# Optimization experiments

Hardware: AMD Instinct MI355X
Metric: run time of the kernel (lower is better)

Reference implementation:

```python
import jax, jax.numpy as jnp
import numpy as np


def _conv1x1(x, w, b=None):
    # x: [B,C,H,W], w: [O,C]
    y = jnp.einsum('bchw,oc->bohw', x, w)
    if b is not None:
        y = y + b[None, :, None, None]
    return y


def _conv3x3_dilated(x, w, b, dil):
    p = dil  # padding == dilation keeps spatial size for 3x3 kernels
    y = jax.lax.conv_general_dilated(
        x, w, window_strides=(1, 1), padding=((p, p), (p, p)),
        rhs_dilation=(dil, dil), dimension_numbers=('NCHW', 'OIHW', 'NCHW'))
    return y + b[None, :, None, None]


def _upsample2x_align_corners(x):
    # bilinear, align_corners=True, scale factor 2
    B, C, H, W = x.shape
    oh, ow = 2 * H, 2 * W
    ys = jnp.linspace(0.0, H - 1.0, oh)
    xs = jnp.linspace(0.0, W - 1.0, ow)
    y0 = jnp.floor(ys).astype(jnp.int32)
    x0 = jnp.floor(xs).astype(jnp.int32)
    y1 = jnp.minimum(y0 + 1, H - 1)
    x1 = jnp.minimum(x0 + 1, W - 1)
    wy = (ys - y0)[None, None, :, None]
    wx = (xs - x0)[None, None, None, :]
    gt = x[:, :, y0, :]
    gb = x[:, :, y1, :]
    top = gt[:, :, :, x0] * (1 - wx) + gt[:, :, :, x1] * wx
    bot = gb[:, :, :, x0] * (1 - wx) + gb[:, :, :, x1] * wx
    return top * (1 - wy) + bot * wy


def _gr(ftr, ck_w, ck_b, avg_w, max_w, gcn_w):
    # GR module: attention-diagonal graph conv with degree normalization
    B, C, H, W = ftr.shape
    HW = H * W
    # ChannelAttention_diag -> diagonal entries cw: [B, M]
    avg = ftr.mean(axis=(2, 3))
    mx = ftr.max(axis=(2, 3))
    cw = jax.nn.sigmoid(jax.nn.relu(avg @ avg_w.T) + jax.nn.relu(mx @ max_w.T))  # [B,M]
    k = jax.nn.relu(_conv1x1(ftr, ck_w, ck_b)).reshape(B, -1, HW)  # [B,M,HW]
    q = jnp.swapaxes(k, 1, 2)  # [B,HW,M]
    # A = sigmoid(q @ diag(cw) @ k); degree d = rowsum(A)^(-1/2)
    A = jax.nn.sigmoid(jnp.einsum('bim,bm,bmj->bij', q, cw, k))  # [B,HW,HW]
    d = A.sum(axis=2) ** -0.5  # [B,HW]
    P = d[:, :, None] * q  # D^{-1/2} @ q, [B,HW,M]
    X = jnp.swapaxes(ftr.reshape(B, C, HW), 1, 2)  # [B,HW,C]
    PtX = jnp.einsum('bjm,bjc->bmc', P, X)  # [B,M,C]
    LX = X - jnp.einsum('bim,bmc->bic', P, cw[:, :, None] * PtX)
    Y = X + LX @ gcn_w  # GCN (no bias)
    return jnp.swapaxes(Y, 1, 2).reshape(B, C, H, W)


def setup_inputs() -> dict:
    key = jax.random.key(0)
    ks = jax.random.split(key, 20)
    B, C = 64, 1024
    Cq = C // 4  # 256
    Mi = Cq // 2  # 128, ChannelAttention inter channels
    s = 0.02
    inp = {
        'x_cur': jax.random.normal(ks[0], (B, C, 16, 16), jnp.float32),
        'x_lat': jax.random.normal(ks[1], (B, C, 8, 8), jnp.float32),
        'conv_w': jax.random.normal(ks[2], (Cq, C), jnp.float32) * s,
        'conv_b': jax.random.normal(ks[3], (Cq,), jnp.float32) * s,
        'conv1_w': jax.random.normal(ks[4], (C, Cq), jnp.float32) * s,
        'conv1_b': jax.random.normal(ks[5], (C,), jnp.float32) * s,
        'conv3_w': jax.random.normal(ks[6], (C, 3 * Cq), jnp.float32) * s,
        'conv3_b': jax.random.normal(ks[7], (C,), jnp.float32) * s,
        'rate0_w': jax.random.normal(ks[8], (Cq, C, 3, 3), jnp.float32) * s,
        'rate0_b': jax.random.normal(ks[9], (Cq,), jnp.float32) * s,
        'rate1_w': jax.random.normal(ks[10], (Cq, C, 3, 3), jnp.float32) * s,
        'rate1_b': jax.random.normal(ks[11], (Cq,), jnp.float32) * s,
        'rate2_w': jax.random.normal(ks[12], (Cq, C, 3, 3), jnp.float32) * s,
        'rate2_b': jax.random.normal(ks[13], (Cq,), jnp.float32) * s,
        'gr_ck_w': jax.random.normal(ks[14], (Mi, Cq), jnp.float32) * s,
        'gr_ck_b': jax.random.normal(ks[15], (Mi,), jnp.float32) * s,
        'gr_avg_w': jax.random.normal(ks[16], (Mi, Cq), jnp.float32) * s,
        'gr_max_w': jax.random.normal(ks[17], (Mi, Cq), jnp.float32) * s,
        'gr_gcn_w': jax.random.normal(ks[18], (Cq, Cq), jnp.float32) * s,
        'pre': 1,
    }
    return inp


def reference(x_cur, x_lat, conv_w, conv_b, conv1_w, conv1_b, conv3_w, conv3_b,
              rate0_w, rate0_b, rate1_w, rate1_b, rate2_w, rate2_b,
              gr_ck_w, gr_ck_b, gr_avg_w, gr_max_w, gr_gcn_w, pre):
    # pre == 1 path of Graph_aspp.forward
    gr_args = (gr_ck_w, gr_ck_b, gr_avg_w, gr_max_w, gr_gcn_w)
    x_sum = x_cur * _upsample2x_align_corners(x_lat) + x_cur
    f1 = _conv3x3_dilated(x_sum, rate0_w, rate0_b, 1) + _conv1x1(x_sum, conv_w, conv_b)
    x1 = _gr(f1, *gr_args)
    feature = _conv1x1(f1, conv1_w, conv1_b) + x_sum
    f2 = _conv3x3_dilated(feature, rate1_w, rate1_b, 2) + _conv1x1(feature, conv_w, conv_b)
    x2 = _gr(f2, *gr_args)
    feature = _conv1x1(f2, conv1_w, conv1_b) + x_sum
    f3 = _conv3x3_dilated(feature, rate2_w, rate2_b, 4) + _conv1x1(feature, conv_w, conv_b)
    x3 = _gr(f3, *gr_args)
    cat = jnp.concatenate((x1, x2, x3), axis=1)
    return _conv1x1(cat, conv3_w, conv3_b)
```

## Files before the change

### kernel.cpp

```cpp
#include <hip/hip_runtime.h>

typedef unsigned short ushort_t;
typedef unsigned int uint32;
typedef __attribute__((ext_vector_type(8))) unsigned short ushort8;
typedef __attribute__((ext_vector_type(8))) __bf16 bf16x8;
typedef __attribute__((ext_vector_type(4))) float f32x4;

__device__ __forceinline__ ushort_t f2b(float f) {
    union { float f; uint32 u; } v; v.f = f;
    uint32 r = v.u + 0x7fffu + ((v.u >> 16) & 1u);
    return (ushort_t)(r >> 16);
}
__device__ __forceinline__ float b2f(ushort_t b) {
    union { uint32 u; float f; } v; v.u = ((uint32)b) << 16;
    return v.f;
}
__device__ __forceinline__ float sigm(float x) { return 1.f / (1.f + __expf(-x)); }

__device__ __forceinline__ void gload_lds16(const void* g, void* l) {
    __builtin_amdgcn_global_load_lds(
        (__attribute__((address_space(1))) void*)g,
        (__attribute__((address_space(3))) void*)l, 16, 0, 0);
}

constexpr int EPI_RELU  = 1;
constexpr int EPI_FEAT  = 2;
constexpr int EPI_SIG   = 3;
constexpr int EPI_XG    = 4;
constexpr int EPI_NEGCW = 5;
constexpr int EPI_Y     = 6;
constexpr int EPI_OUTT  = 7;

struct GemmP {
    const ushort_t* A; const ushort_t* B;
    const ushort_t* A2; const ushort_t* B2;
    long long aBatch, bBatch, a2Batch, b2Batch;
    int lda, ldb, lda2, ldb2;
    int Ksub, kSplit, dil;
    const float* bias;
    const ushort_t* res; long long resBatch; int ldres;
    ushort_t* obf; long long oBatch; int ldo;
    float* of32;
    const float* cw;
    float* dsum;
    const ushort_t* zpage;
};

__global__ __launch_bounds__(256) void gemm_big(GemmP p) {
    __shared__ __align__(16) ushort_t aT[128 * 64];
    __shared__ __align__(16) ushort_t bT[128 * 64];
    const int tid = threadIdx.x;
    const int z = blockIdx.z;
    const int m0 = blockIdx.x * 128, n0 = blockIdx.y * 128;
    const int lane = tid & 63, wid = tid >> 6;
    const int l15 = lane & 15, l16 = lane >> 4;
    const int wr = wid >> 1, wc = wid & 1;
    const int lrow = lane >> 3;
    const int sgran = (lane & 7) ^ lrow;

    int ayy[4], axx[4];
    const ushort_t* aBase[4];
    const ushort_t* bBase[4];
#pragma unroll
    for (int i = 0; i < 4; ++i) {
        int row = wid * 32 + i * 8 + lrow;
        int m = m0 + row;
        int bb = m >> 8;
        ayy[i] = (m >> 4) & 15; axx[i] = m & 15;
        aBase[i] = p.A + (long long)bb * 262144 + sgran * 8;
        bBase[i] = p.B + (long long)(n0 + row) * p.ldb + sgran * 8;
    }

    f32x4 acc[4][4];
#pragma unroll
    for (int i = 0; i < 4; ++i)
#pragma unroll
        for (int j = 0; j < 4; ++j) acc[i][j] = (f32x4){0.f, 0.f, 0.f, 0.f};

    const int gk0 = z * p.kSplit;
    const int iters = p.Ksub >> 6;
    for (int it = 0; it < iters; ++it) {
        const int gk = gk0 + it * 64;
        const int tap = gk >> 10, kin = gk & 1023;
        int dy = 0, dx = 0;
        if (tap < 9) { int ky = tap / 3; dy = (ky - 1) * p.dil; dx = (tap - ky * 3 - 1) * p.dil; }
#pragma unroll
        for (int i = 0; i < 4; ++i) {
            int iy = ayy[i] + dy, ix = axx[i] + dx;
            bool ok = ((unsigned)iy < 16u) && ((unsigned)ix < 16u);
            const ushort_t* ga = ok ? (aBase[i] + (((iy << 4) + ix) << 10) + kin) : p.zpage;
            gload_lds16(ga, &aT[(wid * 32 + i * 8) * 64]);
        }
#pragma unroll
        for (int i = 0; i < 4; ++i)
            gload_lds16(bBase[i] + gk, &bT[(wid * 32 + i * 8) * 64]);
        asm volatile("s_waitcnt vmcnt(0)" ::: "memory");
        __syncthreads();
#pragma unroll
        for (int ks = 0; ks < 2; ++ks) {
            bf16x8 af[4], bfr[4];
#pragma unroll
            for (int mi = 0; mi < 4; ++mi) {
                int rr = wr * 64 + mi * 16 + l15;
                int cc = (ks * 32 + l16 * 8) ^ ((rr & 7) << 3);
                af[mi] = __builtin_bit_cast(bf16x8, *(const ushort8*)&aT[rr * 64 + cc]);
            }
#pragma unroll
            for (int ni = 0; ni < 4; ++ni) {
                int rr = wc * 64 + ni * 16 + l15;
                int cc = (ks * 32 + l16 * 8) ^ ((rr & 7) << 3);
                bfr[ni] = __builtin_bit_cast(bf16x8, *(const ushort8*)&bT[rr * 64 + cc]);
            }
#pragma unroll
            for (int mi = 0; mi < 4; ++mi)
#pragma unroll
                for (int ni = 0; ni < 4; ++ni)
                    acc[mi][ni] = __builtin_amdgcn_mfma_f32_16x16x32_bf16(af[mi], bfr[ni], acc[mi][ni], 0, 0, 0);
        }
        __syncthreads();
    }
#pragma unroll
    for (int mi = 0; mi < 4; ++mi)
#pragma unroll
        for (int ni = 0; ni < 4; ++ni) {
            int gcol = n0 + wc * 64 + ni * 16 + l15;
            int growb = m0 + wr * 64 + mi * 16 + l16 * 4;
#pragma unroll
            for (int r = 0; r < 4; ++r)
                p.obf[(long long)z * p.oBatch + (long long)(growb + r) * 256 + gcol] =
                    f2b(acc[mi][ni][r]);
        }
}

template<int BM, int BN, int AMODE, int EPI>
__global__ __launch_bounds__(256) void gemm_k(GemmP p) {
    __shared__ __align__(16) ushort_t aT[BM * 64];
    __shared__ __align__(16) ushort_t bT[BN * 64];
    constexpr int APASS = BM / 32, BPASS = BN / 32;
    constexpr int MFRAG = BM / 32, NFRAG = BN / 32;
    const int tid = threadIdx.x;
    const int z = blockIdx.z;
    const int m0 = blockIdx.x * BM, n0 = blockIdx.y * BN;
    const int lane = tid & 63, wid = tid >> 6;
    const int l15 = lane & 15, l16 = lane >> 4;
    const int wr = wid >> 1, wc = wid & 1;
    const int srow = tid >> 3, scol = (tid & 7) * 8;
    const int swcol = scol ^ ((srow & 7) << 3);

    const ushort_t* aptr[APASS];
    const ushort_t* bptr[BPASS];
    const ushort_t* aptr2[APASS];
    const ushort_t* bptr2[BPASS];
#pragma unroll
    for (int pi = 0; pi < APASS; ++pi)
        aptr[pi] = p.A + (long long)z * p.aBatch +
                   (long long)(m0 + pi * 32 + srow) * p.lda + scol;
#pragma unroll
    for (int pi = 0; pi < BPASS; ++pi)
        bptr[pi] = p.B + (long long)z * p.bBatch +
                   (long long)(n0 + pi * 32 + srow) * p.ldb + scol;
    if constexpr (AMODE == 2) {
#pragma unroll
        for (int pi = 0; pi < APASS; ++pi)
            aptr2[pi] = p.A2 + (long long)z * p.a2Batch +
                        (long long)(m0 + pi * 32 + srow) * p.lda2 + scol;
#pragma unroll
        for (int pi = 0; pi < BPASS; ++pi)
            bptr2[pi] = p.B2 + (long long)z * p.b2Batch +
                        (long long)(n0 + pi * 32 + srow) * p.ldb2 + scol;
    }

    f32x4 acc[MFRAG][NFRAG];
#pragma unroll
    for (int i = 0; i < MFRAG; ++i)
#pragma unroll
        for (int j = 0; j < NFRAG; ++j) acc[i][j] = (f32x4){0.f, 0.f, 0.f, 0.f};

    ushort8 ar[APASS], br[BPASS];
    auto ldg = [&](int gk) {
        if (AMODE == 2 && gk >= 256) {
            int g2 = gk - 256;
#pragma unroll
            for (int pi = 0; pi < APASS; ++pi) ar[pi] = *(const ushort8*)(aptr2[pi] + g2);
#pragma unroll
            for (int pi = 0; pi < BPASS; ++pi) br[pi] = *(const ushort8*)(bptr2[pi] + g2);
        } else if constexpr (AMODE == 3) {
#pragma unroll
            for (int pi = 0; pi < APASS; ++pi) {
                ushort8 t8 = *(const ushort8*)(aptr[pi] + gk);
#pragma unroll
                for (int k = 0; k < 8; ++k)
                    t8[k] = f2b(b2f(t8[k]) * p.cw[(z << 7) + gk + scol + k]);
                ar[pi] = t8;
            }
#pragma unroll
            for (int pi = 0; pi < BPASS; ++pi) br[pi] = *(const ushort8*)(bptr[pi] + gk);
        } else {
#pragma unroll
            for (int pi = 0; pi < APASS; ++pi) ar[pi] = *(const ushort8*)(aptr[pi] + gk);
#pragma unroll
            for (int pi = 0; pi < BPASS; ++pi) br[pi] = *(const ushort8*)(bptr[pi] + gk);
        }
    };

    const int gk0 = z * p.kSplit;
    ldg(gk0);
    const int iters = p.Ksub >> 6;
    for (int it = 0; it < iters; ++it) {
#pragma unroll
        for (int pi = 0; pi < APASS; ++pi)
            *(ushort8*)&aT[(pi * 32 + srow) * 64 + swcol] = ar[pi];
#pragma unroll
        for (int pi = 0; pi < BPASS; ++pi)
            *(ushort8*)&bT[(pi * 32 + srow) * 64 + swcol] = br[pi];
        __syncthreads();
        if (it + 1 < iters) ldg(gk0 + (it + 1) * 64);
#pragma unroll
        for (int ks = 0; ks < 2; ++ks) {
            bf16x8 af[MFRAG], bfr[NFRAG];
#pragma unroll
            for (int mi = 0; mi < MFRAG; ++mi) {
                int rr = wr * (BM / 2) + mi * 16 + l15;
                int cc = (ks * 32 + l16 * 8) ^ ((rr & 7) << 3);
                af[mi] = __builtin_bit_cast(bf16x8, *(const ushort8*)&aT[rr * 64 + cc]);
            }
#pragma unroll
            for (int ni = 0; ni < NFRAG; ++ni) {
                int rr = wc * (BN / 2) + ni * 16 + l15;
                int cc = (ks * 32 + l16 * 8) ^ ((rr & 7) << 3);
                bfr[ni] = __builtin_bit_cast(bf16x8, *(const ushort8*)&bT[rr * 64 + cc]);
            }
#pragma unroll
            for (int mi = 0; mi < MFRAG; ++mi)
#pragma unroll
                for (int ni = 0; ni < NFRAG; ++ni)
                    acc[mi][ni] = __builtin_amdgcn_mfma_f32_16x16x32_bf16(af[mi], bfr[ni], acc[mi][ni], 0, 0, 0);
        }
        __syncthreads();
    }

#pragma unroll
    for (int mi = 0; mi < MFRAG; ++mi) {
        if constexpr (EPI == EPI_SIG) {
#pragma unroll
            for (int r = 0; r < 4; ++r) {
                float sv = 0.f;
#pragma unroll
                for (int ni = 0; ni < NFRAG; ++ni) sv += sigm(acc[mi][ni][r]);
                sv += __shfl_xor(sv, 1); sv += __shfl_xor(sv, 2);
                sv += __shfl_xor(sv, 4); sv += __shfl_xor(sv, 8);
                if (l15 == 0) {
                    int grow = m0 + wr * (BM / 2) + mi * 16 + l16 * 4 + r;
                    int q8 = blockIdx.y * 2 + wc;
                    p.dsum[q8 * 16384 + z * 256 + grow] = sv;
                }
            }
        } else {
#pragma unroll
            for (int ni = 0; ni < NFRAG; ++ni) {
                int gcol = n0 + wc * (BN / 2) + ni * 16 + l15;
                int growb = m0 + wr * (BM / 2) + mi * 16 + l16 * 4;
#pragma unroll
                for (int r = 0; r < 4; ++r) {
                    int grow = growb + r;
                    float v = acc[mi][ni][r];
                    if constexpr (EPI == EPI_RELU) {
                        v += p.bias[gcol]; v = fmaxf(v, 0.f);
                        p.obf[(long long)grow * p.ldo + gcol] = f2b(v);
                    } else if constexpr (EPI == EPI_FEAT) {
                        v += p.bias[gcol] + b2f(p.res[(long long)grow * p.ldres + gcol]);
                        p.obf[(long long)grow * p.ldo + gcol] = f2b(v);
                    } else if constexpr (EPI == EPI_XG) {
                        p.obf[(long long)z * p.oBatch + (long long)grow * p.ldo + gcol] = f2b(v);
                    } else if constexpr (EPI == EPI_NEGCW) {
                        v *= -p.cw[z * 128 + gcol];
                        p.obf[(long long)z * p.oBatch + (long long)grow * p.ldo + gcol] = f2b(v);
                    } else if constexpr (EPI == EPI_Y) {
                        v = b2f(p.res[(long long)z * p.resBatch + (long long)grow * p.ldres + gcol]) + v;
                        p.obf[(long long)z * p.oBatch + (long long)grow * p.ldo + gcol] = f2b(v);
                    } else if constexpr (EPI == EPI_OUTT) {
                        v += p.bias[grow];
                        int bb = gcol >> 8, px = gcol & 255;
                        p.of32[((long long)bb * 1024 + grow) * 256 + px] = v;
                    }
                }
            }
        }
    }
}


__global__ void k_combine(const ushort_t* __restrict__ t, const float* __restrict__ fbias_s,
                          ushort_t* __restrict__ f) {
    int idx = blockIdx.x * 256 + threadIdx.x;
    const long long N = 16384ll * 256;
    ushort8 a0 = *(const ushort8*)(t + (long long)idx * 8);
    ushort8 a1 = *(const ushort8*)(t + N + (long long)idx * 8);
    ushort8 a2 = *(const ushort8*)(t + 2 * N + (long long)idx * 8);
    ushort8 a3 = *(const ushort8*)(t + 3 * N + (long long)idx * 8);
    ushort8 a4 = *(const ushort8*)(t + 4 * N + (long long)idx * 8);
    int cb = (idx * 8) & 255;
    ushort8 o;
#pragma unroll
    for (int k = 0; k < 8; ++k)
        o[k] = f2b(b2f(a0[k]) + b2f(a1[k]) + b2f(a2[k]) + b2f(a3[k]) + b2f(a4[k]) + fbias_s[cb + k]);
    *(ushort8*)&f[(long long)idx * 8] = o;
}

__global__ void k_upsum(const float* __restrict__ xc, const float* __restrict__ xl,
                        ushort_t* __restrict__ xs) {
    __shared__ float lat[64 * 64];
    __shared__ ushort_t tile[64 * 258];
    int b = blockIdx.x, c0 = blockIdx.y * 64;
    int t = threadIdx.x;
    for (int i = t; i < 4096; i += 256)
        lat[i] = xl[((long long)(b * 1024 + c0 + (i >> 6))) * 64 + (i & 63)];
    __syncthreads();
    int y = t >> 4, x = t & 15;
    float fy = y * (7.f / 15.f); int y0 = (int)fy; float wy = fy - y0; int y1 = y0 + 1 > 7 ? 7 : y0 + 1;
    float fx = x * (7.f / 15.f); int x0 = (int)fx; float wx = fx - x0; int x1 = x0 + 1 > 7 ? 7 : x0 + 1;
    for (int cc = 0; cc < 64; ++cc) {
        float cur = xc[((long long)(b * 1024 + c0 + cc)) * 256 + t];
        const float* L = &lat[cc * 64];
        float tv = L[y0 * 8 + x0] * (1.f - wx) + L[y0 * 8 + x1] * wx;
        float bv = L[y1 * 8 + x0] * (1.f - wx) + L[y1 * 8 + x1] * wx;
        float up = tv + (bv - tv) * wy;
        tile[cc * 258 + t] = f2b(cur * (1.f + up));
    }
    __syncthreads();
    for (int i = t; i < 16384; i += 256) {
        int px = i >> 6, cc = i & 63;
        xs[((long long)(b * 256 + px)) * 1024 + c0 + cc] = tile[cc * 258 + px];
    }
}

__global__ void k_poolcw(const ushort_t* __restrict__ f,
                         const float* __restrict__ aw, const float* __restrict__ mw,
                         float* __restrict__ cw) {
    __shared__ float sa[256], sm[256];
    int b = blockIdx.x, t = threadIdx.x;
    float s = 0.f, m = -3.4e38f;
    const ushort_t* base = f + (long long)b * 65536 + t;
    for (int px = 0; px < 256; ++px) { float v = b2f(base[px * 256]); s += v; m = fmaxf(m, v); }
    sa[t] = s * (1.f / 256.f);
    sm[t] = m;
    __syncthreads();
    if (t < 128) {
        float s1 = 0.f, s2 = 0.f;
        const float* a = aw + t * 256; const float* w = mw + t * 256;
        for (int c = 0; c < 256; ++c) { s1 += sa[c] * a[c]; s2 += sm[c] * w[c]; }
        s1 = fmaxf(s1, 0.f); s2 = fmaxf(s2, 0.f);
        cw[b * 128 + t] = sigm(s1 + s2);
    }
}

__global__ void k_pscale(const ushort_t* __restrict__ q, const float* __restrict__ dsum8,
                         ushort_t* __restrict__ P, ushort_t* __restrict__ Pt) {
    __shared__ ushort_t t[128][130];
    __shared__ float dd[128];
    int jh = blockIdx.x, b = blockIdx.y;
    int j0 = jh * 128;
    int tid = threadIdx.x;
    if (tid < 128) {
        int pix = b * 256 + j0 + tid;
        float s = 0.f;
#pragma unroll
        for (int qs = 0; qs < 8; ++qs) s += dsum8[qs * 16384 + pix];
        dd[tid] = rsqrtf(s);
    }
    __syncthreads();
    int jr = tid >> 7, m = tid & 127;
    for (int i = 0; i < 64; ++i) {
        int j = i * 2 + jr;
        long long qi = ((long long)(b * 256 + j0 + j)) * 128 + m;
        ushort_t v = f2b(dd[j] * b2f(q[qi]));
        P[qi] = v;
        t[j][m] = v;
    }
    __syncthreads();
    for (int i = 0; i < 64; ++i) {
        int mm = i * 2 + jr;
        Pt[((long long)b << 15) + (mm << 8) + j0 + m] = t[m][mm];
    }
}

__global__ void k_packall(const float* r0, const float* r1, const float* r2,
                          const float* convw, const float* c1w, const float* c3w,
                          const float* ckw, const float* gcnw,
                          const float* rb0, const float* rb1, const float* rb2,
                          const float* cb,
                          ushort_t* wbig3, ushort_t* w1b, ushort_t* w3b,
                          ushort_t* ckb, ushort_t* gcnT, float* fbias,
                          ushort_t* zpage) {
    int blk = blockIdx.x, tid = threadIdx.x;
    if (blk < 768) {
        __shared__ float lw[10240];
        int s = blk >> 8, o = blk & 255;
        const float* rate = s == 0 ? r0 : (s == 1 ? r1 : r2);
        for (int i = tid; i < 9216; i += 256) lw[i] = rate[(long long)o * 9216 + i];
        for (int i = tid; i < 1024; i += 256) lw[9216 + i] = convw[(long long)o * 1024 + i];
        __syncthreads();
        ushort_t* dst = wbig3 + (long long)blk * 10240;
        for (int i = tid; i < 10240; i += 256) {
            int tap = i >> 10, ci = i & 1023;
            float v = (tap < 9) ? lw[ci * 9 + tap] : lw[9216 + ci];
            dst[i] = f2b(v);
        }
        return;
    }
    const int R1 = 262144, R2 = R1 + 786432, R3 = R2 + 32768, R4 = R3 + 65536;
    const int R5 = R4 + 768, R6 = R5 + 128;
    int base = (blk - 768) * 2048 + tid * 8;
#pragma unroll
    for (int k = 0; k < 8; ++k) {
        int i = base + k;
        if (i >= R6) return;
        if (i < R1) w1b[i] = f2b(c1w[i]);
        else if (i < R2) w3b[i - R1] = f2b(c3w[i - R1]);
        else if (i < R3) ckb[i - R2] = f2b(ckw[i - R2]);
        else if (i < R4) {
            int ii = i - R3; int c2 = ii >> 8, c1 = ii & 255;
            gcnT[ii] = f2b(gcnw[c1 * 256 + c2]);
        } else if (i < R5) {
            int ii = i - R4; int s = ii >> 8, t = ii & 255;
            const float* rb = s == 0 ? rb0 : (s == 1 ? rb1 : rb2);
            fbias[ii] = rb[t] + cb[t];
        } else {
            zpage[i - R5] = 0;
        }
    }
}

__global__ void k_sentinel(float* o, int n, float v) {
    int i = blockIdx.x * 256 + threadIdx.x; if (i < n) o[i] = v;
}

extern "C" void kernel_launch(void* const* d_in, const int* in_sizes, int n_in,
                              void* d_out, int out_size, void* d_ws, size_t ws_size,
                              hipStream_t stream) {
    const float* x_cur  = (const float*)d_in[0];
    const float* x_lat  = (const float*)d_in[1];
    const float* conv_w = (const float*)d_in[2];
    const float* conv_b = (const float*)d_in[3];
    const float* conv1_w = (const float*)d_in[4];
    const float* conv1_b = (const float*)d_in[5];
    const float* conv3_w = (const float*)d_in[6];
    const float* conv3_b = (const float*)d_in[7];
    const float* rate_w[3] = {(const float*)d_in[8], (const float*)d_in[10], (const float*)d_in[12]};
    const float* rate_b[3] = {(const float*)d_in[9], (const float*)d_in[11], (const float*)d_in[13]};
    const float* ck_w  = (const float*)d_in[14];
    const float* ck_b  = (const float*)d_in[15];
    const float* avg_w = (const float*)d_in[16];
    const float* max_w = (const float*)d_in[17];
    const float* gcn_w = (const float*)d_in[18];
    float* out = (float*)d_out;

    char* w = (char*)d_ws;
    auto take = [&](size_t bytes) { void* p = (void*)w; w += (bytes + 255) & ~(size_t)255; return p; };
    ushort_t* xsum  = (ushort_t*)take(16384ll * 1024 * 2);
    ushort_t* feat  = (ushort_t*)take(16384ll * 1024 * 2);
    ushort_t* fbuf  = (ushort_t*)take(16384ll * 256 * 2);
    ushort_t* xgt   = (ushort_t*)take(64ll * 256 * 256 * 2);
    ushort_t* qbuf  = (ushort_t*)take(16384ll * 128 * 2);
    ushort_t* Pt    = (ushort_t*)take(64ll * 128 * 256 * 2);
    ushort_t* Pb    = (ushort_t*)take(16384ll * 128 * 2);
    ushort_t* Htn   = (ushort_t*)take(64ll * 256 * 128 * 2);
    ushort_t* wbig3 = (ushort_t*)take(3ll * 256 * 10240 * 2);
    ushort_t* w1b   = (ushort_t*)take(1024ll * 256 * 2);
    ushort_t* w3b   = (ushort_t*)take(1024ll * 768 * 2);
    ushort_t* ckb   = (ushort_t*)take(128ll * 256 * 2);
    ushort_t* gcnT  = (ushort_t*)take(256ll * 256 * 2);
    ushort_t* zpage = (ushort_t*)take(256);
    float*    fbias = (float*)take(3 * 256 * 4);
    float*    cwb   = (float*)take(64 * 128 * 4);
    float*    dsum8 = (float*)take(8ll * 64 * 256 * 4);
    ushort_t* catb  = (ushort_t*)take(16384ll * 768 * 2);
    ushort_t* ftmp  = (ushort_t*)take(5ll * 16384 * 256 * 2);
    size_t need = (size_t)(w - (char*)d_ws);

    if (need > ws_size) {
        float v = 1.0e6f + (float)(ws_size >> 20);
        k_sentinel<<<(out_size + 255) / 256, 256, 0, stream>>>(out, out_size, v);
        return;
    }

    k_packall<<<768 + 561, 256, 0, stream>>>(
        rate_w[0], rate_w[1], rate_w[2], conv_w, conv1_w, conv3_w, ck_w, gcn_w,
        rate_b[0], rate_b[1], rate_b[2], conv_b,
        wbig3, w1b, w3b, ckb, gcnT, fbias, zpage);
    k_upsum<<<dim3(64, 16), 256, 0, stream>>>(x_cur, x_lat, xsum);

    for (int s = 0; s < 3; ++s) {
        {
            GemmP p{};
            p.A = (s == 0) ? xsum : feat;
            p.B = wbig3 + (long long)s * 256 * 10240; p.ldb = 10240;
            p.Ksub = 2048; p.kSplit = 2048; p.dil = 1 << s;
            p.obf = ftmp; p.oBatch = 16384ll * 256;
            p.zpage = zpage;
            gemm_big<<<dim3(128, 2, 5), 256, 0, stream>>>(p);
        }
        k_combine<<<2048, 256, 0, stream>>>(ftmp, fbias + s * 256, fbuf);
        k_poolcw<<<64, 256, 0, stream>>>(fbuf, avg_w, max_w, cwb);
        {
            GemmP p{};
            p.A = fbuf; p.lda = 256; p.B = ckb; p.ldb = 256;
            p.Ksub = 256;
            p.bias = ck_b; p.obf = qbuf; p.ldo = 128;
            gemm_k<64, 64, 0, EPI_RELU><<<dim3(256, 2, 1), 256, 0, stream>>>(p);
        }
        {
            GemmP p{};
            p.A = qbuf; p.aBatch = 32768; p.lda = 128;
            p.B = qbuf; p.bBatch = 32768; p.ldb = 128;
            p.Ksub = 128; p.dsum = dsum8; p.cw = cwb;
            gemm_k<64, 64, 3, EPI_SIG><<<dim3(4, 4, 64), 256, 0, stream>>>(p);
        }
        k_pscale<<<dim3(2, 64), 256, 0, stream>>>(qbuf, dsum8, Pb, Pt);
        {
            GemmP p{};
            p.A = gcnT; p.aBatch = 0;     p.lda = 256;
            p.B = fbuf; p.bBatch = 65536; p.ldb = 256;
            p.Ksub = 256;
            p.obf = xgt; p.oBatch = 65536; p.ldo = 256;
            gemm_k<64, 64, 0, EPI_XG><<<dim3(4, 4, 64), 256, 0, stream>>>(p);
        }
        {
            GemmP p{};
            p.A = xgt; p.aBatch = 65536; p.lda = 256;
            p.B = Pt;  p.bBatch = 32768; p.ldb = 256;
            p.Ksub = 256; p.cw = cwb;
            p.obf = Htn; p.oBatch = 32768; p.ldo = 128;
            gemm_k<64, 64, 0, EPI_NEGCW><<<dim3(4, 2, 64), 256, 0, stream>>>(p);
        }
        {
            GemmP p{};
            p.A = fbuf; p.aBatch = 65536; p.lda = 256;
            p.B = gcnT; p.bBatch = 0;     p.ldb = 256;
            p.A2 = Pb;  p.a2Batch = 32768; p.lda2 = 128;
            p.B2 = Htn; p.b2Batch = 32768; p.ldb2 = 128;
            p.Ksub = 384;
            p.res = fbuf; p.resBatch = 65536; p.ldres = 256;
            p.obf = catb + s * 256; p.oBatch = 256ll * 768; p.ldo = 768;
            gemm_k<64, 64, 2, EPI_Y><<<dim3(4, 4, 64), 256, 0, stream>>>(p);
        }
        if (s < 2) {
            GemmP p{};
            p.A = fbuf; p.lda = 256; p.B = w1b; p.ldb = 256;
            p.Ksub = 256; p.bias = conv1_b;
            p.res = xsum; p.ldres = 1024;
            p.obf = feat; p.ldo = 1024;
            gemm_k<64, 64, 0, EPI_FEAT><<<dim3(256, 16, 1), 256, 0, stream>>>(p);
        }
    }
    {
        GemmP p{};
        p.A = w3b;  p.lda = 768;
        p.B = catb; p.ldb = 768;
        p.Ksub = 768; p.bias = conv3_b; p.of32 = out;
        gemm_k<128, 128, 0, EPI_OUTT><<<dim3(8, 128, 1), 256, 0, stream>>>(p);
    }
}
```

Measured before the change: 696.1 us.

## Hoist tap addressing in conv GEMM, drop P buffer, widen pooling and FEAT tiles

The dilated-conv GEMM now computes per-tap A/B base addresses once per 1024-wide tap, with an inner 16-step K loop. The zero page is enlarged so swizzled offsets stay in bounds. k_pscale no longer writes the scaled P matrix. Instead it stores per-pixel degree scales, and the Y GEMM rescales q rows while loading, which removes one buffer write and read. k_poolcw uses 1024 threads with a 4-way reduction, and the FEAT GEMM switches to a 64x128 tile.

```diff
diff --git a/kernel.cpp b/kernel.cpp
--- a/kernel.cpp
+++ b/kernel.cpp
@@ -42,6 +42,7 @@
     ushort_t* obf; long long oBatch; int ldo;
     float* of32;
     const float* cw;
+    const float* rscale;
     float* dsum;
     const ushort_t* zpage;
 };
@@ -78,46 +79,53 @@
         for (int j = 0; j < 4; ++j) acc[i][j] = (f32x4){0.f, 0.f, 0.f, 0.f};
 
     const int gk0 = z * p.kSplit;
-    const int iters = p.Ksub >> 6;
-    for (int it = 0; it < iters; ++it) {
-        const int gk = gk0 + it * 64;
-        const int tap = gk >> 10, kin = gk & 1023;
+    const int ntap = p.Ksub >> 10;
+    for (int ti = 0; ti < ntap; ++ti) {
+        const int tap = (gk0 >> 10) + ti;
         int dy = 0, dx = 0;
         if (tap < 9) { int ky = tap / 3; dy = (ky - 1) * p.dil; dx = (tap - ky * 3 - 1) * p.dil; }
+        const ushort_t* gaA[4];
+        const ushort_t* gaB[4];
 #pragma unroll
         for (int i = 0; i < 4; ++i) {
             int iy = ayy[i] + dy, ix = axx[i] + dx;
             bool ok = ((unsigned)iy < 16u) && ((unsigned)ix < 16u);
-            const ushort_t* ga = ok ? (aBase[i] + (((iy << 4) + ix) << 10) + kin) : p.zpage;
-            gload_lds16(ga, &aT[(wid * 32 + i * 8) * 64]);
-        }
-#pragma unroll
-        for (int i = 0; i < 4; ++i)
-            gload_lds16(bBase[i] + gk, &bT[(wid * 32 + i * 8) * 64]);
-        asm volatile("s_waitcnt vmcnt(0)" ::: "memory");
-        __syncthreads();
-#pragma unroll
-        for (int ks = 0; ks < 2; ++ks) {
-            bf16x8 af[4], bfr[4];
-#pragma unroll
-            for (int mi = 0; mi < 4; ++mi) {
-                int rr = wr * 64 + mi * 16 + l15;
-                int cc = (ks * 32 + l16 * 8) ^ ((rr & 7) << 3);
-                af[mi] = __builtin_bit_cast(bf16x8, *(const ushort8*)&aT[rr * 64 + cc]);
-            }
-#pragma unroll
-            for (int ni = 0; ni < 4; ++ni) {
-                int rr = wc * 64 + ni * 16 + l15;
-                int cc = (ks * 32 + l16 * 8) ^ ((rr & 7) << 3);
-                bfr[ni] = __builtin_bit_cast(bf16x8, *(const ushort8*)&bT[rr * 64 + cc]);
-            }
-#pragma unroll
-            for (int mi = 0; mi < 4; ++mi)
-#pragma unroll
-                for (int ni = 0; ni < 4; ++ni)
-                    acc[mi][ni] = __builtin_amdgcn_mfma_f32_16x16x32_bf16(af[mi], bfr[ni], acc[mi][ni], 0, 0, 0);
-        }
-        __syncthreads();
+            gaA[i] = ok ? (aBase[i] + (((iy << 4) + ix) << 10)) : (p.zpage + sgran * 8);
+            gaB[i] = bBase[i] + (tap << 10);
+        }
+        for (int kk = 0; kk < 16; ++kk) {
+            const int kin = kk << 6;
+#pragma unroll
+            for (int i = 0; i < 4; ++i)
+                gload_lds16(gaA[i] + kin, &aT[(wid * 32 + i * 8) * 64]);
+#pragma unroll
+            for (int i = 0; i < 4; ++i)
+                gload_lds16(gaB[i] + kin, &bT[(wid * 32 + i * 8) * 64]);
+            asm volatile("s_waitcnt vmcnt(0)" ::: "memory");
+            __syncthreads();
+#pragma unroll
+            for (int ks = 0; ks < 2; ++ks) {
+                bf16x8 af[4], bfr[4];
+#pragma unroll
+                for (int mi = 0; mi < 4; ++mi) {
+                    int rr = wr * 64 + mi * 16 + l15;
+                    int cc = (ks * 32 + l16 * 8) ^ ((rr & 7) << 3);
+                    af[mi] = __builtin_bit_cast(bf16x8, *(const ushort8*)&aT[rr * 64 + cc]);
+                }
+#pragma unroll
+                for (int ni = 0; ni < 4; ++ni) {
+                    int rr = wc * 64 + ni * 16 + l15;
+                    int cc = (ks * 32 + l16 * 8) ^ ((rr & 7) << 3);
+                    bfr[ni] = __builtin_bit_cast(bf16x8, *(const ushort8*)&bT[rr * 64 + cc]);
+                }
+#pragma unroll
+                for (int mi = 0; mi < 4; ++mi)
+#pragma unroll
+                    for (int ni = 0; ni < 4; ++ni)
+                        acc[mi][ni] = __builtin_amdgcn_mfma_f32_16x16x32_bf16(af[mi], bfr[ni], acc[mi][ni], 0, 0, 0);
+            }
+            __syncthreads();
+        }
     }
 #pragma unroll
     for (int mi = 0; mi < 4; ++mi)
@@ -151,6 +159,7 @@
     const ushort_t* bptr[BPASS];
     const ushort_t* aptr2[APASS];
     const ushort_t* bptr2[BPASS];
+    float rsA[APASS];
 #pragma unroll
     for (int pi = 0; pi < APASS; ++pi)
         aptr[pi] = p.A + (long long)z * p.aBatch +
@@ -161,9 +170,11 @@
                    (long long)(n0 + pi * 32 + srow) * p.ldb + scol;
     if constexpr (AMODE == 2) {
 #pragma unroll
-        for (int pi = 0; pi < APASS; ++pi)
+        for (int pi = 0; pi < APASS; ++pi) {
             aptr2[pi] = p.A2 + (long long)z * p.a2Batch +
                         (long long)(m0 + pi * 32 + srow) * p.lda2 + scol;
+            rsA[pi] = p.rscale[z * 256 + m0 + pi * 32 + srow];
+        }
 #pragma unroll
         for (int pi = 0; pi < BPASS; ++pi)
             bptr2[pi] = p.B2 + (long long)z * p.b2Batch +
@@ -181,7 +192,12 @@
         if (AMODE == 2 && gk >= 256) {
             int g2 = gk - 256;
 #pragma unroll
-            for (int pi = 0; pi < APASS; ++pi) ar[pi] = *(const ushort8*)(aptr2[pi] + g2);
+            for (int pi = 0; pi < APASS; ++pi) {
+                ushort8 t8 = *(const ushort8*)(aptr2[pi] + g2);
+#pragma unroll
+                for (int k = 0; k < 8; ++k) t8[k] = f2b(b2f(t8[k]) * rsA[pi]);
+                ar[pi] = t8;
+            }
 #pragma unroll
             for (int pi = 0; pi < BPASS; ++pi) br[pi] = *(const ushort8*)(bptr2[pi] + g2);
         } else if constexpr (AMODE == 3) {
@@ -337,25 +353,35 @@
 __global__ void k_poolcw(const ushort_t* __restrict__ f,
                          const float* __restrict__ aw, const float* __restrict__ mw,
                          float* __restrict__ cw) {
-    __shared__ float sa[256], sm[256];
+    __shared__ float ss[4][256];
+    __shared__ float mm_[4][256];
     int b = blockIdx.x, t = threadIdx.x;
+    int ch = t & 255, grp = t >> 8;
     float s = 0.f, m = -3.4e38f;
-    const ushort_t* base = f + (long long)b * 65536 + t;
-    for (int px = 0; px < 256; ++px) { float v = b2f(base[px * 256]); s += v; m = fmaxf(m, v); }
-    sa[t] = s * (1.f / 256.f);
-    sm[t] = m;
+    const ushort_t* base = f + (long long)b * 65536 + ch;
+    for (int px = grp; px < 256; px += 4) {
+        float v = b2f(base[px * 256]); s += v; m = fmaxf(m, v);
+    }
+    ss[grp][ch] = s; mm_[grp][ch] = m;
+    __syncthreads();
+    if (t < 256) {
+        s = ss[0][t] + ss[1][t] + ss[2][t] + ss[3][t];
+        m = fmaxf(fmaxf(mm_[0][t], mm_[1][t]), fmaxf(mm_[2][t], mm_[3][t]));
+        ss[0][t] = s * (1.f / 256.f);
+        mm_[0][t] = m;
+    }
     __syncthreads();
     if (t < 128) {
         float s1 = 0.f, s2 = 0.f;
         const float* a = aw + t * 256; const float* w = mw + t * 256;
-        for (int c = 0; c < 256; ++c) { s1 += sa[c] * a[c]; s2 += sm[c] * w[c]; }
+        for (int c = 0; c < 256; ++c) { s1 += ss[0][c] * a[c]; s2 += mm_[0][c] * w[c]; }
         s1 = fmaxf(s1, 0.f); s2 = fmaxf(s2, 0.f);
         cw[b * 128 + t] = sigm(s1 + s2);
     }
 }
 
 __global__ void k_pscale(const ushort_t* __restrict__ q, const float* __restrict__ dsum8,
-                         ushort_t* __restrict__ P, ushort_t* __restrict__ Pt) {
+                         float* __restrict__ dscale, ushort_t* __restrict__ Pt) {
     __shared__ ushort_t t[128][130];
     __shared__ float dd[128];
     int jh = blockIdx.x, b = blockIdx.y;
@@ -366,16 +392,16 @@
         float s = 0.f;
 #pragma unroll
         for (int qs = 0; qs < 8; ++qs) s += dsum8[qs * 16384 + pix];
-        dd[tid] = rsqrtf(s);
+        float r = rsqrtf(s);
+        dd[tid] = r;
+        dscale[pix] = r;
     }
     __syncthreads();
     int jr = tid >> 7, m = tid & 127;
     for (int i = 0; i < 64; ++i) {
         int j = i * 2 + jr;
         long long qi = ((long long)(b * 256 + j0 + j)) * 128 + m;
-        ushort_t v = f2b(dd[j] * b2f(q[qi]));
-        P[qi] = v;
-        t[j][m] = v;
+        t[j][m] = f2b(dd[j] * b2f(q[qi]));
     }
     __syncthreads();
     for (int i = 0; i < 64; ++i) {
@@ -409,7 +435,7 @@
         return;
     }
     const int R1 = 262144, R2 = R1 + 786432, R3 = R2 + 32768, R4 = R3 + 65536;
-    const int R5 = R4 + 768, R6 = R5 + 128;
+    const int R5 = R4 + 768, R6 = R5 + 4096;
     int base = (blk - 768) * 2048 + tid * 8;
 #pragma unroll
     for (int k = 0; k < 8; ++k) {
@@ -457,25 +483,25 @@
 
     char* w = (char*)d_ws;
     auto take = [&](size_t bytes) { void* p = (void*)w; w += (bytes + 255) & ~(size_t)255; return p; };
-    ushort_t* xsum  = (ushort_t*)take(16384ll * 1024 * 2);
-    ushort_t* feat  = (ushort_t*)take(16384ll * 1024 * 2);
-    ushort_t* fbuf  = (ushort_t*)take(16384ll * 256 * 2);
-    ushort_t* xgt   = (ushort_t*)take(64ll * 256 * 256 * 2);
-    ushort_t* qbuf  = (ushort_t*)take(16384ll * 128 * 2);
-    ushort_t* Pt    = (ushort_t*)take(64ll * 128 * 256 * 2);
-    ushort_t* Pb    = (ushort_t*)take(16384ll * 128 * 2);
-    ushort_t* Htn   = (ushort_t*)take(64ll * 256 * 128 * 2);
-    ushort_t* wbig3 = (ushort_t*)take(3ll * 256 * 10240 * 2);
-    ushort_t* w1b   = (ushort_t*)take(1024ll * 256 * 2);
-    ushort_t* w3b   = (ushort_t*)take(1024ll * 768 * 2);
-    ushort_t* ckb   = (ushort_t*)take(128ll * 256 * 2);
-    ushort_t* gcnT  = (ushort_t*)take(256ll * 256 * 2);
-    ushort_t* zpage = (ushort_t*)take(256);
-    float*    fbias = (float*)take(3 * 256 * 4);
-    float*    cwb   = (float*)take(64 * 128 * 4);
-    float*    dsum8 = (float*)take(8ll * 64 * 256 * 4);
-    ushort_t* catb  = (ushort_t*)take(16384ll * 768 * 2);
-    ushort_t* ftmp  = (ushort_t*)take(5ll * 16384 * 256 * 2);
+    ushort_t* xsum   = (ushort_t*)take(16384ll * 1024 * 2);
+    ushort_t* feat   = (ushort_t*)take(16384ll * 1024 * 2);
+    ushort_t* fbuf   = (ushort_t*)take(16384ll * 256 * 2);
+    ushort_t* xgt    = (ushort_t*)take(64ll * 256 * 256 * 2);
+    ushort_t* qbuf   = (ushort_t*)take(16384ll * 128 * 2);
+    ushort_t* Pt     = (ushort_t*)take(64ll * 128 * 256 * 2);
+    ushort_t* Htn    = (ushort_t*)take(64ll * 256 * 128 * 2);
+    ushort_t* wbig3  = (ushort_t*)take(3ll * 256 * 10240 * 2);
+    ushort_t* w1b    = (ushort_t*)take(1024ll * 256 * 2);
+    ushort_t* w3b    = (ushort_t*)take(1024ll * 768 * 2);
+    ushort_t* ckb    = (ushort_t*)take(128ll * 256 * 2);
+    ushort_t* gcnT   = (ushort_t*)take(256ll * 256 * 2);
+    ushort_t* zpage  = (ushort_t*)take(8192);
+    float*    fbias  = (float*)take(3 * 256 * 4);
+    float*    cwb    = (float*)take(64 * 128 * 4);
+    float*    dscale = (float*)take(64 * 256 * 4);
+    float*    dsum8  = (float*)take(8ll * 64 * 256 * 4);
+    ushort_t* catb   = (ushort_t*)take(16384ll * 768 * 2);
+    ushort_t* ftmp   = (ushort_t*)take(5ll * 16384 * 256 * 2);
     size_t need = (size_t)(w - (char*)d_ws);
 
     if (need > ws_size) {
@@ -484,7 +510,7 @@
         return;
     }
 
-    k_packall<<<768 + 561, 256, 0, stream>>>(
+    k_packall<<<768 + 563, 256, 0, stream>>>(
         rate_w[0], rate_w[1], rate_w[2], conv_w, conv1_w, conv3_w, ck_w, gcn_w,
         rate_b[0], rate_b[1], rate_b[2], conv_b,
         wbig3, w1b, w3b, ckb, gcnT, fbias, zpage);
@@ -501,7 +527,7 @@
             gemm_big<<<dim3(128, 2, 5), 256, 0, stream>>>(p);
         }
         k_combine<<<2048, 256, 0, stream>>>(ftmp, fbias + s * 256, fbuf);
-        k_poolcw<<<64, 256, 0, stream>>>(fbuf, avg_w, max_w, cwb);
+        k_poolcw<<<64, 1024, 0, stream>>>(fbuf, avg_w, max_w, cwb);
         {
             GemmP p{};
             p.A = fbuf; p.lda = 256; p.B = ckb; p.ldb = 256;
@@ -516,7 +542,7 @@
             p.Ksub = 128; p.dsum = dsum8; p.cw = cwb;
             gemm_k<64, 64, 3, EPI_SIG><<<dim3(4, 4, 64), 256, 0, stream>>>(p);
         }
-        k_pscale<<<dim3(2, 64), 256, 0, stream>>>(qbuf, dsum8, Pb, Pt);
+        k_pscale<<<dim3(2, 64), 256, 0, stream>>>(qbuf, dsum8, dscale, Pt);
         {
             GemmP p{};
             p.A = gcnT; p.aBatch = 0;     p.lda = 256;
@@ -537,8 +563,8 @@
             GemmP p{};
             p.A = fbuf; p.aBatch = 65536; p.lda = 256;
             p.B = gcnT; p.bBatch = 0;     p.ldb = 256;
-            p.A2 = Pb;  p.a2Batch = 32768; p.lda2 = 128;
-            p.B2 = Htn; p.b2Batch = 32768; p.ldb2 = 128;
+            p.A2 = qbuf; p.a2Batch = 32768; p.lda2 = 128; p.rscale = dscale;
+            p.B2 = Htn;  p.b2Batch = 32768; p.ldb2 = 128;
             p.Ksub = 384;
             p.res = fbuf; p.resBatch = 65536; p.ldres = 256;
             p.obf = catb + s * 256; p.oBatch = 256ll * 768; p.ldo = 768;
@@ -550,7 +576,7 @@
             p.Ksub = 256; p.bias = conv1_b;
             p.res = xsum; p.ldres = 1024;
             p.obf = feat; p.ldo = 1024;
-            gemm_k<64, 64, 0, EPI_FEAT><<<dim3(256, 16, 1), 256, 0, stream>>>(p);
+            gemm_k<64, 128, 0, EPI_FEAT><<<dim3(256, 8, 1), 256, 0, stream>>>(p);
         }
     }
     {
```

Measured after the change: 707.3 us. About the same (+1.6%).
